# Kernel optimization log

Measured on AMD Instinct MI355X. Metric: run time of the kernel, lower is better.

The kernel has to match this reference:

```python
import jax, jax.numpy as jnp
import numpy as np

N = 50000      # nodes
E = 800000     # edges (avg degree 16)
IN = 128       # in_channels
H = 256        # hidden_channels
EPS = 1e-5     # BatchNorm eps


def setup_inputs() -> dict:
    key = jax.random.key(0)
    ks = iter(jax.random.split(key, 40))
    nrm = lambda shape, s: jax.random.normal(next(ks), shape, dtype=jnp.float32) * s
    d = {}
    d["x"] = nrm((N, IN), 1.0)
    d["edge_index"] = jax.random.randint(next(ks), (2, E), 0, N, dtype=jnp.int32)
    # SAGEConv layers: lin_l (neighbors, with bias) + lin_r (root, no bias); BatchNorm params
    dims = [(IN, H), (H, H), (H, H)]
    for i, (fi, fo) in enumerate(dims):
        s = 1.0 / np.sqrt(fi)
        d[f"w_l{i}"] = nrm((fo, fi), s)
        d[f"b_l{i}"] = nrm((fo,), s)
        d[f"w_r{i}"] = nrm((fo, fi), s)
        d[f"g{i}"] = jnp.ones((fo,), jnp.float32)
        d[f"be{i}"] = nrm((fo,), 0.1)
        d[f"rm{i}"] = nrm((fo,), 0.1)
        d[f"rv{i}"] = jax.random.uniform(next(ks), (fo,), jnp.float32, 0.5, 1.5)
    # predictor MLP: H->H, H->H//2, H//2->1
    for j, (fi, fo) in enumerate([(H, H), (H, H // 2), (H // 2, 1)], start=1):
        s = 1.0 / np.sqrt(fi)
        d[f"pw{j}"] = nrm((fo, fi), s)
        d[f"pb{j}"] = nrm((fo,), s)
    return d


def _sage(x, src, dst, w_l, b_l, w_r):
    # mean aggregation of neighbor messages (gather by src, scatter-add by dst)
    msum = jax.ops.segment_sum(x[src], dst, num_segments=N)       # [N, F]
    cnt = jax.ops.segment_sum(jnp.ones((src.shape[0], 1), x.dtype), dst, num_segments=N)
    mean = msum / jnp.maximum(cnt, 1.0)
    return mean @ w_l.T + b_l + x @ w_r.T


def _bn(x, g, be, rm, rv):
    return (x - rm) * jax.lax.rsqrt(rv + EPS) * g + be


def reference(x, edge_index,
              w_l0, b_l0, w_r0, g0, be0, rm0, rv0,
              w_l1, b_l1, w_r1, g1, be1, rm1, rv1,
              w_l2, b_l2, w_r2, g2, be2, rm2, rv2,
              pw1, pb1, pw2, pb2, pw3, pb3):
    src, dst = edge_index[0], edge_index[1]
    layers = [
        (w_l0, b_l0, w_r0, g0, be0, rm0, rv0),
        (w_l1, b_l1, w_r1, g1, be1, rm1, rv1),
        (w_l2, b_l2, w_r2, g2, be2, rm2, rv2),
    ]
    for (wl, bl, wr, g, be, rm, rv) in layers:
        x = _sage(x, src, dst, wl, bl, wr)
        x = jax.nn.relu(_bn(x, g, be, rm, rv))
        # dropout: identity in eval mode
    h = jax.nn.relu(x @ pw1.T + pb1)
    h = jax.nn.relu(h @ pw2.T + pb2)
    return jax.nn.sigmoid(h @ pw3.T + pb3)   # [N, 1]
```

## Files before the change

### kernel.cpp

```cpp
#include <hip/hip_runtime.h>
#include <hip/hip_fp16.h>

#define NNODES 50000
#define NEDGES 800000

typedef _Float16 f16;
typedef f16 f16x8 __attribute__((ext_vector_type(8)));
typedef f16 f16x4 __attribute__((ext_vector_type(4)));
typedef float f32x4 __attribute__((ext_vector_type(4)));

#define GLOAD_LDS16(g, l) __builtin_amdgcn_global_load_lds( \
    (const __attribute__((address_space(1))) void*)(g), \
    (__attribute__((address_space(3))) void*)(l), 16, 0, 0)


__global__ void k_deg(const int* __restrict__ dst, int* __restrict__ deg, int E) {
    int i = blockIdx.x * blockDim.x + threadIdx.x;
    int stride = gridDim.x * blockDim.x;
    for (; i < E; i += stride) atomicAdd(&deg[dst[i]], 1);
}

__global__ void k_bsum(const int* __restrict__ deg, int* __restrict__ bsum, int n) {
    __shared__ int s[256];
    int i = blockIdx.x * 256 + threadIdx.x;
    s[threadIdx.x] = (i < n) ? ((deg[i] + 7) & ~7) : 0;
    __syncthreads();
    for (int off = 128; off; off >>= 1) {
        if (threadIdx.x < off) s[threadIdx.x] += s[threadIdx.x + off];
        __syncthreads();
    }
    if (threadIdx.x == 0) bsum[blockIdx.x] = s[0];
}

__global__ void k_scan_bsum(int* __restrict__ bsum, int nb) {
    int lane = threadIdx.x & 63;
    int carry = 0;
    for (int base = 0; base < nb; base += 64) {
        int i = base + lane;
        int v = (i < nb) ? bsum[i] : 0;
        int orig = v;
        for (int off = 1; off < 64; off <<= 1) {
            int x = __shfl_up(v, off);
            if (lane >= off) v += x;
        }
        if (i < nb) bsum[i] = carry + v - orig;
        carry += __shfl(v, 63);
    }
}

__global__ void k_offsets(const int* __restrict__ deg, const int* __restrict__ bsum,
                          int* __restrict__ offs, int n) {
    __shared__ int s[256];
    int t = threadIdx.x;
    int i = blockIdx.x * 256 + t;
    int v = (i < n) ? ((deg[i] + 7) & ~7) : 0;
    s[t] = v;
    __syncthreads();
    for (int off = 1; off < 256; off <<= 1) {
        int x = (t >= off) ? s[t - off] : 0;
        __syncthreads();
        s[t] += x;
        __syncthreads();
    }
    if (i < n) offs[i] = bsum[blockIdx.x] + s[t] - v;
    if (i == n - 1) offs[n] = bsum[blockIdx.x] + s[t];
}

__global__ void k_scatter_pad(const int* __restrict__ src, const int* __restrict__ dst,
                              const int* __restrict__ offs, const int* __restrict__ deg,
                              int* __restrict__ cursor, int* __restrict__ csr,
                              int E, int n) {
    int i = blockIdx.x * blockDim.x + threadIdx.x;
    int stride = gridDim.x * blockDim.x;
    for (int e = i; e < E; e += stride) {
        int d = dst[e];
        int p = atomicAdd(&cursor[d], 1);
        csr[offs[d] + p] = src[e];
    }
    for (int v = i; v < n; v += stride) {
        int d = deg[v], pd = (d + 7) & ~7;
        int base = offs[v];
        for (int p = d; p < pd; ++p) csr[base + p] = NNODES;
    }
}


__global__ void k_prep(const float* __restrict__ x, f16* __restrict__ h0, int n4,
                       const float* __restrict__ pw3, f16* __restrict__ pw3f,
                       f16* __restrict__ hA, f16* __restrict__ hB) {
    int gid0 = blockIdx.x * blockDim.x + threadIdx.x;
    int gstride = gridDim.x * blockDim.x;
    for (int i = gid0; i < n4; i += gstride) {
        float4 v = ((const float4*)x)[i];
        f16x4 o;
        o[0] = (f16)v.x; o[1] = (f16)v.y; o[2] = (f16)v.z; o[3] = (f16)v.w;
        ((f16x4*)h0)[i] = o;
    }
    f16x4 z = {};
    if (gid0 < 32) {
        ((f16x4*)(h0 + (size_t)NNODES * 128))[gid0] = z;
    } else if (gid0 < 96) {
        ((f16x4*)(hA + (size_t)NNODES * 256))[gid0 - 32] = z;
    } else if (gid0 < 160) {
        ((f16x4*)(hB + (size_t)NNODES * 256))[gid0 - 96] = z;
    } else if (gid0 < 192) {
        int i = gid0 - 160;
        float4 v = ((const float4*)pw3)[i];
        f16x4 o;
        o[0] = (f16)v.x; o[1] = (f16)v.y; o[2] = (f16)v.z; o[3] = (f16)v.w;
        ((f16x4*)pw3f)[i] = o;
    }
}


#define NPK 8
struct PackSeg { const float* w; f16* p; int FO; int K; };
struct PackArgs { PackSeg s[NPK]; };

__global__ void k_packw(PackArgs a) {
    int gid = blockIdx.x * blockDim.x + threadIdx.x;
    int gstride = gridDim.x * blockDim.x;
    for (int sgi = 0; sgi < NPK; ++sgi) {
        PackSeg sg = a.s[sgi];
        int total = sg.FO * sg.K / 8;
        int KS = sg.K >> 5;
        for (int t = gid; t < total; t += gstride) {
            int lane = t & 63;
            int tile = t >> 6;
            int ks = tile % KS, nt = tile / KS;
            int row = nt * 16 + (lane & 15);
            int col = ks * 32 + (lane >> 4) * 8;
            const float4* src = (const float4*)(sg.w + (size_t)row * sg.K + col);
            float4 v0 = src[0], v1 = src[1];
            f16x8 o;
            o[0] = (f16)v0.x; o[1] = (f16)v0.y; o[2] = (f16)v0.z; o[3] = (f16)v0.w;
            o[4] = (f16)v1.x; o[5] = (f16)v1.y; o[6] = (f16)v1.z; o[7] = (f16)v1.w;
            ((f16x8*)sg.p)[t] = o;
        }
    }
}


struct AffSeg { const float *b, *g, *be, *rm, *rv; float *cs, *cb; int n; int isbn; };
struct AffArgs { AffSeg s[5]; };

__global__ void k_affine_all(AffArgs a) {
    AffSeg sg = a.s[blockIdx.x];
    int t = threadIdx.x;
    if (t < sg.n) {
        if (sg.isbn) {
            float sc = sg.g[t] * rsqrtf(sg.rv[t] + 1e-5f);
            sg.cs[t] = sc;
            sg.cb[t] = (sg.b[t] - sg.rm[t]) * sc + sg.be[t];
        } else {
            sg.cs[t] = 1.0f;
            sg.cb[t] = sg.b[t];
        }
    }
}

template <int F>
__global__ __launch_bounds__(256) void k_aggregate(
    const f16* __restrict__ h, const int* __restrict__ poffs,
    const int* __restrict__ deg, const int* __restrict__ csr,
    f16* __restrict__ mean) {
    constexpr int LPN = F / 8;
    constexpr int NPW = 64 / LPN;
    int tid = threadIdx.x;
    int wave = tid >> 6, lane = tid & 63;
    int node = blockIdx.x * (4 * NPW) + wave * NPW + lane / LPN;
    int t = lane % LPN;
    int beg = poffs[node], end = poffs[node + 1];
    int nb = (end - beg) >> 3;
    const f16x8* hb = (const f16x8*)h;
    float acc[8] = {0.f, 0.f, 0.f, 0.f, 0.f, 0.f, 0.f, 0.f};

    int j = beg;
    for (int p = 0; p + 2 <= nb; p += 2, j += 16) {
        int iA[8], iB[8];
#pragma unroll
        for (int u = 0; u < 8; ++u) iA[u] = csr[j + u];
#pragma unroll
        for (int u = 0; u < 8; ++u) iB[u] = csr[j + 8 + u];
        f16x8 vA[8], vB[8];
#pragma unroll
        for (int u = 0; u < 8; ++u) vA[u] = hb[(size_t)iA[u] * LPN + t];
#pragma unroll
        for (int u = 0; u < 8; ++u) vB[u] = hb[(size_t)iB[u] * LPN + t];
#pragma unroll
        for (int u = 0; u < 8; ++u)
#pragma unroll
            for (int e = 0; e < 8; ++e) acc[e] += (float)vA[u][e];
#pragma unroll
        for (int u = 0; u < 8; ++u)
#pragma unroll
            for (int e = 0; e < 8; ++e) acc[e] += (float)vB[u][e];
    }
    if (nb & 1) {
        int iA[8];
#pragma unroll
        for (int u = 0; u < 8; ++u) iA[u] = csr[j + u];
        f16x8 vA[8];
#pragma unroll
        for (int u = 0; u < 8; ++u) vA[u] = hb[(size_t)iA[u] * LPN + t];
#pragma unroll
        for (int u = 0; u < 8; ++u)
#pragma unroll
            for (int e = 0; e < 8; ++e) acc[e] += (float)vA[u][e];
    }

    int d = deg[node];
    float inv = (d > 0) ? 1.0f / (float)d : 0.0f;
    f16x8 o;
#pragma unroll
    for (int e = 0; e < 8; ++e) o[e] = (f16)(acc[e] * inv);
    ((f16x8*)mean)[(size_t)node * LPN + t] = o;
}

template <int FO, bool FUSE>
__global__ __launch_bounds__(FO * 2, 4) void k_gemm(
    const f16* __restrict__ A1, const f16* __restrict__ A2,
    const f16* __restrict__ W1p, const f16* __restrict__ W2p,
    const float* __restrict__ cs, const float* __restrict__ cb,
    f16* __restrict__ out, const f16* __restrict__ w3,
    const float* __restrict__ pb3, float* __restrict__ outF,
    int M, int K) {
    constexpr int WC = FO / 64;
    constexpr int NT = FO * 2;
    __shared__ f16 As[2][128 * 64];
    __shared__ float smF[WC][128];
    int tid = threadIdx.x;
    int lane = tid & 63;
    int wave = tid >> 6;
    int wr = wave / WC, wc = wave % WC;
    int m0 = blockIdx.x * 128;
    int lrow = lane & 15;
    int kof8 = (lane >> 4) * 8;
    int KC1 = K >> 6;
    int KS = K >> 5;
    int NC = A2 ? KC1 * 2 : KC1;

    auto stage = [&](int buf, int c) {
        int ph = (c >= KC1) ? 1 : 0;
        const char* Ab = (const char*)(ph ? A2 : A1);
        int kb0 = ((c - ph * KC1) << 6) * 2;
        char* Al = (char*)&As[buf][0];
#pragma unroll
        for (int u0 = 0; u0 < 1024; u0 += NT) {
            int u = u0 + tid;
            int row = u >> 3;
            int kb = (u & 7) * 16;
            int grow = m0 + row; if (grow > M - 1) grow = M - 1;
            GLOAD_LDS16(Ab + (size_t)grow * (K * 2) + kb0 + (kb ^ ((row & 7) << 4)), Al + u * 16);
        }
    };

    f32x4 acc[4][4] = {};

    stage(0, 0);
    __syncthreads();

    for (int c = 0; c < NC; ++c) {
        int ph = (c >= KC1) ? 1 : 0;
        const f16x8* Wp = (const f16x8*)(ph ? W2p : W1p);
        int cl = c - ph * KC1;
        f16x8 b[2][4];
#pragma unroll
        for (int kk = 0; kk < 2; ++kk) {
            int ks = cl * 2 + kk;
#pragma unroll
            for (int ni = 0; ni < 4; ++ni) {
                int nt = wc * 4 + ni;
                b[kk][ni] = Wp[((size_t)nt * KS + ks) * 64 + lane];
            }
        }
        if (c + 1 < NC) stage((c + 1) & 1, c + 1);
        const char* Al = (const char*)&As[c & 1][0];
#pragma unroll
        for (int kk = 0; kk < 2; ++kk) {
            int kb = kof8 * 2 + kk * 64;
            f16x8 a[4];
#pragma unroll
            for (int mi = 0; mi < 4; ++mi) {
                int r = wr * 64 + mi * 16 + lrow;
                a[mi] = *(const f16x8*)(Al + r * 128 + (kb ^ ((r & 7) << 4)));
            }
#pragma unroll
            for (int mi = 0; mi < 4; ++mi)
#pragma unroll
                for (int ni = 0; ni < 4; ++ni)
                    acc[mi][ni] = __builtin_amdgcn_mfma_f32_16x16x32_f16(a[mi], b[kk][ni], acc[mi][ni], 0, 0, 0);
        }
        __syncthreads();
    }

    if constexpr (!FUSE) {
        int rquad = (lane >> 4) * 4;
#pragma unroll
        for (int mi = 0; mi < 4; ++mi) {
#pragma unroll
            for (int ni = 0; ni < 4; ++ni) {
                int col = wc * 64 + ni * 16 + (lane & 15);
                float s = cs[col], cc = cb[col];
#pragma unroll
                for (int r = 0; r < 4; ++r) {
                    int row = m0 + wr * 64 + mi * 16 + rquad + r;
                    if (row < M) {
                        float v = acc[mi][ni][r] * s + cc;
                        v = fmaxf(v, 0.f);
                        out[(size_t)row * FO + col] = (f16)v;
                    }
                }
            }
        }
    } else {
        float b3 = pb3[0];
        float rsum[4][4] = {};
#pragma unroll
        for (int ni = 0; ni < 4; ++ni) {
            int col = wc * 64 + ni * 16 + (lane & 15);
            float w3v = (float)w3[col];
            float cbv = cb[col];
#pragma unroll
            for (int mi = 0; mi < 4; ++mi)
#pragma unroll
                for (int r = 0; r < 4; ++r)
                    rsum[mi][r] += fmaxf(acc[mi][ni][r] + cbv, 0.f) * w3v;
        }
#pragma unroll
        for (int mi = 0; mi < 4; ++mi)
#pragma unroll
            for (int r = 0; r < 4; ++r) {
                float s = rsum[mi][r];
                s += __shfl_xor(s, 1); s += __shfl_xor(s, 2);
                s += __shfl_xor(s, 4); s += __shfl_xor(s, 8);
                if ((lane & 15) == 0)
                    smF[wc][wr * 64 + mi * 16 + (lane >> 4) * 4 + r] = s;
            }
        __syncthreads();
        if (tid < 128) {
            int row = m0 + tid;
            if (row < M) {
                float s = b3;
#pragma unroll
                for (int w = 0; w < WC; ++w) s += smF[w][tid];
                outF[row] = 1.0f / (1.0f + expf(-s));
            }
        }
    }
}


extern "C" void kernel_launch(void* const* d_in, const int* in_sizes, int n_in,
                              void* d_out, int out_size, void* d_ws, size_t ws_size,
                              hipStream_t stream) {
    const float* x = (const float*)d_in[0];
    const int* ei = (const int*)d_in[1];
    const int* src = ei;
    const int* dst = ei + NEDGES;
    const float* w_l[3] = {(const float*)d_in[2], (const float*)d_in[9], (const float*)d_in[16]};
    const float* b_l[3] = {(const float*)d_in[3], (const float*)d_in[10], (const float*)d_in[17]};
    const float* w_r[3] = {(const float*)d_in[4], (const float*)d_in[11], (const float*)d_in[18]};
    const float* g[3]  = {(const float*)d_in[5], (const float*)d_in[12], (const float*)d_in[19]};
    const float* be[3] = {(const float*)d_in[6], (const float*)d_in[13], (const float*)d_in[20]};
    const float* rm[3] = {(const float*)d_in[7], (const float*)d_in[14], (const float*)d_in[21]};
    const float* rv[3] = {(const float*)d_in[8], (const float*)d_in[15], (const float*)d_in[22]};
    const float* pw1 = (const float*)d_in[23]; const float* pb1 = (const float*)d_in[24];
    const float* pw2 = (const float*)d_in[25]; const float* pb2 = (const float*)d_in[26];
    const float* pw3 = (const float*)d_in[27]; const float* pb3 = (const float*)d_in[28];

    char* wsb = (char*)d_ws;
    size_t o = 0;
    auto alloc = [&](size_t b) { size_t r = o; o = (o + b + 255) & ~(size_t)255; return r; };

    size_t deg_off = alloc(NNODES * 4);
    size_t cur_off = alloc(NNODES * 4);
    int* deg    = (int*)(wsb + deg_off);
    int* cursor = (int*)(wsb + cur_off);
    int* poffs  = (int*)(wsb + alloc((NNODES + 1) * 4));
    int* bsum   = (int*)(wsb + alloc(256 * 4));
    int* csr    = (int*)(wsb + alloc((NEDGES + 8 * NNODES) * 4));
    f16* h0   = (f16*)(wsb + alloc((size_t)(NNODES + 1) * 128 * 2));
    f16* hA   = (f16*)(wsb + alloc((size_t)(NNODES + 1) * 256 * 2));
    f16* hB   = (f16*)(wsb + alloc((size_t)(NNODES + 1) * 256 * 2));
    f16* mean = (f16*)(wsb + alloc((size_t)NNODES * 256 * 2));
    f16* wl0p = (f16*)(wsb + alloc(256 * 128 * 2));
    f16* wr0p = (f16*)(wsb + alloc(256 * 128 * 2));
    f16* wl1p = (f16*)(wsb + alloc(256 * 256 * 2));
    f16* wr1p = (f16*)(wsb + alloc(256 * 256 * 2));
    f16* wl2p = (f16*)(wsb + alloc(256 * 256 * 2));
    f16* wr2p = (f16*)(wsb + alloc(256 * 256 * 2));
    f16* pw1p = (f16*)(wsb + alloc(256 * 256 * 2));
    f16* pw2p = (f16*)(wsb + alloc(128 * 256 * 2));
    f16* pw3f = (f16*)(wsb + alloc(128 * 2));
    float* csv[5]; float* cbv[5];
    for (int i = 0; i < 5; ++i) {
        csv[i] = (float*)(wsb + alloc(256 * 4));
        cbv[i] = (float*)(wsb + alloc(256 * 4));
    }

    hipMemsetAsync(wsb + deg_off, 0, cur_off - deg_off + NNODES * 4, stream);
    k_deg<<<3125, 256, 0, stream>>>(dst, deg, NEDGES);
    int nb = (NNODES + 255) / 256;
    k_bsum<<<nb, 256, 0, stream>>>(deg, bsum, NNODES);
    k_scan_bsum<<<1, 64, 0, stream>>>(bsum, nb);
    k_offsets<<<nb, 256, 0, stream>>>(deg, bsum, poffs, NNODES);
    k_scatter_pad<<<3125, 256, 0, stream>>>(src, dst, poffs, deg, cursor, csr, NEDGES, NNODES);

    k_prep<<<1600, 256, 0, stream>>>(x, h0, NNODES * 128 / 4, pw3, pw3f, hA, hB);
    PackArgs pa;
    pa.s[0] = {w_l[0], wl0p, 256, 128};
    pa.s[1] = {w_r[0], wr0p, 256, 128};
    pa.s[2] = {w_l[1], wl1p, 256, 256};
    pa.s[3] = {w_r[1], wr1p, 256, 256};
    pa.s[4] = {w_l[2], wl2p, 256, 256};
    pa.s[5] = {w_r[2], wr2p, 256, 256};
    pa.s[6] = {pw1,    pw1p, 256, 256};
    pa.s[7] = {pw2,    pw2p, 128, 256};
    k_packw<<<64, 256, 0, stream>>>(pa);

    AffArgs aa;
    for (int i = 0; i < 3; ++i)
        aa.s[i] = {b_l[i], g[i], be[i], rm[i], rv[i], csv[i], cbv[i], 256, 1};
    aa.s[3] = {pb1, nullptr, nullptr, nullptr, nullptr, csv[3], cbv[3], 256, 0};
    aa.s[4] = {pb2, nullptr, nullptr, nullptr, nullptr, csv[4], cbv[4], 128, 0};
    k_affine_all<<<5, 256, 0, stream>>>(aa);

    int gm = (NNODES + 127) / 128;

    k_aggregate<128><<<3125, 256, 0, stream>>>(h0, poffs, deg, csr, mean);
    k_gemm<256, false><<<gm, 512, 0, stream>>>(mean, h0, wl0p, wr0p, csv[0], cbv[0], hA,
                                               nullptr, nullptr, nullptr, NNODES, 128);
    k_aggregate<256><<<6250, 256, 0, stream>>>(hA, poffs, deg, csr, mean);
    k_gemm<256, false><<<gm, 512, 0, stream>>>(mean, hA, wl1p, wr1p, csv[1], cbv[1], hB,
                                               nullptr, nullptr, nullptr, NNODES, 256);
    k_aggregate<256><<<6250, 256, 0, stream>>>(hB, poffs, deg, csr, mean);
    k_gemm<256, false><<<gm, 512, 0, stream>>>(mean, hB, wl2p, wr2p, csv[2], cbv[2], hA,
                                               nullptr, nullptr, nullptr, NNODES, 256);
    k_gemm<256, false><<<gm, 512, 0, stream>>>(hA, nullptr, pw1p, nullptr, csv[3], cbv[3], hB,
                                               nullptr, nullptr, nullptr, NNODES, 256);
    k_gemm<128, true><<<gm, 256, 0, stream>>>(hB, nullptr, pw2p, nullptr, csv[4], cbv[4], nullptr,
                                              pw3f, pb3, (float*)d_out, NNODES, 256);
}
```

Measured before the change: 347.0 us.

## Fuse preprocessing kernels into one launch and split 256-wide GEMMs across two blocks

The degree count, input cast, weight packing, BN affine folding and padding-row init now run in a single k_front launch, with each role picked by block index. This removes several small kernel launches. The FO=256 GEMMs now use 256-thread blocks, each covering 128 output columns, so the grid doubles to about 782 blocks for better CU occupancy. The cost is that each A tile is now loaded into LDS twice, once per column half.

```diff
diff --git a/kernel.cpp b/kernel.cpp
--- a/kernel.cpp
+++ b/kernel.cpp
@@ -13,12 +13,6 @@
     (const __attribute__((address_space(1))) void*)(g), \
     (__attribute__((address_space(3))) void*)(l), 16, 0, 0)
 
-
-__global__ void k_deg(const int* __restrict__ dst, int* __restrict__ deg, int E) {
-    int i = blockIdx.x * blockDim.x + threadIdx.x;
-    int stride = gridDim.x * blockDim.x;
-    for (; i < E; i += stride) atomicAdd(&deg[dst[i]], 1);
-}
 
 __global__ void k_bsum(const int* __restrict__ deg, int* __restrict__ bsum, int n) {
     __shared__ int s[256];
@@ -85,76 +79,78 @@
 }
 
 
-__global__ void k_prep(const float* __restrict__ x, f16* __restrict__ h0, int n4,
-                       const float* __restrict__ pw3, f16* __restrict__ pw3f,
-                       f16* __restrict__ hA, f16* __restrict__ hB) {
-    int gid0 = blockIdx.x * blockDim.x + threadIdx.x;
-    int gstride = gridDim.x * blockDim.x;
-    for (int i = gid0; i < n4; i += gstride) {
-        float4 v = ((const float4*)x)[i];
-        f16x4 o;
-        o[0] = (f16)v.x; o[1] = (f16)v.y; o[2] = (f16)v.z; o[3] = (f16)v.w;
-        ((f16x4*)h0)[i] = o;
-    }
-    f16x4 z = {};
-    if (gid0 < 32) {
-        ((f16x4*)(h0 + (size_t)NNODES * 128))[gid0] = z;
-    } else if (gid0 < 96) {
-        ((f16x4*)(hA + (size_t)NNODES * 256))[gid0 - 32] = z;
-    } else if (gid0 < 160) {
-        ((f16x4*)(hB + (size_t)NNODES * 256))[gid0 - 96] = z;
-    } else if (gid0 < 192) {
-        int i = gid0 - 160;
-        float4 v = ((const float4*)pw3)[i];
-        f16x4 o;
-        o[0] = (f16)v.x; o[1] = (f16)v.y; o[2] = (f16)v.z; o[3] = (f16)v.w;
-        ((f16x4*)pw3f)[i] = o;
-    }
-}
-
-
 #define NPK 8
 struct PackSeg { const float* w; f16* p; int FO; int K; };
-struct PackArgs { PackSeg s[NPK]; };
-
-__global__ void k_packw(PackArgs a) {
-    int gid = blockIdx.x * blockDim.x + threadIdx.x;
-    int gstride = gridDim.x * blockDim.x;
-    for (int sgi = 0; sgi < NPK; ++sgi) {
-        PackSeg sg = a.s[sgi];
-        int total = sg.FO * sg.K / 8;
-        int KS = sg.K >> 5;
-        for (int t = gid; t < total; t += gstride) {
-            int lane = t & 63;
-            int tile = t >> 6;
-            int ks = tile % KS, nt = tile / KS;
-            int row = nt * 16 + (lane & 15);
-            int col = ks * 32 + (lane >> 4) * 8;
-            const float4* src = (const float4*)(sg.w + (size_t)row * sg.K + col);
-            float4 v0 = src[0], v1 = src[1];
-            f16x8 o;
-            o[0] = (f16)v0.x; o[1] = (f16)v0.y; o[2] = (f16)v0.z; o[3] = (f16)v0.w;
-            o[4] = (f16)v1.x; o[5] = (f16)v1.y; o[6] = (f16)v1.z; o[7] = (f16)v1.w;
-            ((f16x8*)sg.p)[t] = o;
-        }
-    }
-}
-
-
 struct AffSeg { const float *b, *g, *be, *rm, *rv; float *cs, *cb; int n; int isbn; };
-struct AffArgs { AffSeg s[5]; };
-
-__global__ void k_affine_all(AffArgs a) {
-    AffSeg sg = a.s[blockIdx.x];
-    int t = threadIdx.x;
-    if (t < sg.n) {
-        if (sg.isbn) {
-            float sc = sg.g[t] * rsqrtf(sg.rv[t] + 1e-5f);
-            sg.cs[t] = sc;
-            sg.cb[t] = (sg.b[t] - sg.rm[t]) * sc + sg.be[t];
-        } else {
-            sg.cs[t] = 1.0f;
-            sg.cb[t] = sg.b[t];
+
+struct FrontArgs {
+    const int* dst; int* deg;
+    const float* x; f16* h0; int n4;
+    const float* pw3; f16* pw3f;
+    f16 *hA, *hB;
+    PackSeg ps[NPK];
+    AffSeg as[5];
+};
+
+__global__ void k_front(FrontArgs a) {
+    int b = blockIdx.x, tid = threadIdx.x;
+    if (b < 1024) {
+        int i = b * 256 + tid, stride = 1024 * 256;
+        for (; i < NEDGES; i += stride) atomicAdd(&a.deg[a.dst[i]], 1);
+    } else if (b < 2624) {
+        int i = (b - 1024) * 256 + tid, stride = 1600 * 256;
+        for (; i < a.n4; i += stride) {
+            float4 v = ((const float4*)a.x)[i];
+            f16x4 o;
+            o[0] = (f16)v.x; o[1] = (f16)v.y; o[2] = (f16)v.z; o[3] = (f16)v.w;
+            ((f16x4*)a.h0)[i] = o;
+        }
+    } else if (b < 2880) {
+        int gid = (b - 2624) * 256 + tid, gstride = 256 * 256;
+        for (int sgi = 0; sgi < NPK; ++sgi) {
+            PackSeg sg = a.ps[sgi];
+            int total = sg.FO * sg.K / 8;
+            int KS = sg.K >> 5;
+            for (int t = gid; t < total; t += gstride) {
+                int lane = t & 63;
+                int tile = t >> 6;
+                int ks = tile % KS, nt = tile / KS;
+                int row = nt * 16 + (lane & 15);
+                int col = ks * 32 + (lane >> 4) * 8;
+                const float4* srcp = (const float4*)(sg.w + (size_t)row * sg.K + col);
+                float4 v0 = srcp[0], v1 = srcp[1];
+                f16x8 o;
+                o[0] = (f16)v0.x; o[1] = (f16)v0.y; o[2] = (f16)v0.z; o[3] = (f16)v0.w;
+                o[4] = (f16)v1.x; o[5] = (f16)v1.y; o[6] = (f16)v1.z; o[7] = (f16)v1.w;
+                ((f16x8*)sg.p)[t] = o;
+            }
+        }
+    } else if (b < 2885) {
+        AffSeg sg = a.as[b - 2880];
+        if (tid < sg.n) {
+            if (sg.isbn) {
+                float sc = sg.g[tid] * rsqrtf(sg.rv[tid] + 1e-5f);
+                sg.cs[tid] = sc;
+                sg.cb[tid] = (sg.b[tid] - sg.rm[tid]) * sc + sg.be[tid];
+            } else {
+                sg.cs[tid] = 1.0f;
+                sg.cb[tid] = sg.b[tid];
+            }
+        }
+    } else {
+        f16x4 z = {};
+        if (tid < 32) {
+            ((f16x4*)(a.h0 + (size_t)NNODES * 128))[tid] = z;
+        } else if (tid < 96) {
+            ((f16x4*)(a.hA + (size_t)NNODES * 256))[tid - 32] = z;
+        } else if (tid < 160) {
+            ((f16x4*)(a.hB + (size_t)NNODES * 256))[tid - 96] = z;
+        } else if (tid < 192) {
+            int i = tid - 160;
+            float4 v = ((const float4*)a.pw3)[i];
+            f16x4 o;
+            o[0] = (f16)v.x; o[1] = (f16)v.y; o[2] = (f16)v.z; o[3] = (f16)v.w;
+            ((f16x4*)a.pw3f)[i] = o;
         }
     }
 }
@@ -217,16 +213,105 @@
     ((f16x8*)mean)[(size_t)node * LPN + t] = o;
 }
 
-template <int FO, bool FUSE>
-__global__ __launch_bounds__(FO * 2, 4) void k_gemm(
+__global__ __launch_bounds__(256, 4) void k_gemm2(
     const f16* __restrict__ A1, const f16* __restrict__ A2,
     const f16* __restrict__ W1p, const f16* __restrict__ W2p,
     const float* __restrict__ cs, const float* __restrict__ cb,
-    f16* __restrict__ out, const f16* __restrict__ w3,
+    f16* __restrict__ out, int M, int K) {
+    __shared__ f16 As[2][128 * 64];
+    int tid = threadIdx.x;
+    int lane = tid & 63;
+    int wave = tid >> 6;
+    int wr = wave >> 1, wc = wave & 1;
+    int m0 = (blockIdx.x >> 1) * 128;
+    int nb0 = (blockIdx.x & 1) * 128;
+    int lrow = lane & 15;
+    int kof8 = (lane >> 4) * 8;
+    int KC1 = K >> 6;
+    int KS = K >> 5;
+    int NC = A2 ? KC1 * 2 : KC1;
+
+    auto stage = [&](int buf, int c) {
+        int ph = (c >= KC1) ? 1 : 0;
+        const char* Ab = (const char*)(ph ? A2 : A1);
+        int kb0 = ((c - ph * KC1) << 6) * 2;
+        char* Al = (char*)&As[buf][0];
+#pragma unroll
+        for (int u0 = 0; u0 < 1024; u0 += 256) {
+            int u = u0 + tid;
+            int row = u >> 3;
+            int kb = (u & 7) * 16;
+            int grow = m0 + row; if (grow > M - 1) grow = M - 1;
+            GLOAD_LDS16(Ab + (size_t)grow * (K * 2) + kb0 + (kb ^ ((row & 7) << 4)), Al + u * 16);
+        }
+    };
+
+    f32x4 acc[4][4] = {};
+
+    stage(0, 0);
+    __syncthreads();
+
+    for (int c = 0; c < NC; ++c) {
+        int ph = (c >= KC1) ? 1 : 0;
+        const f16x8* Wp = (const f16x8*)(ph ? W2p : W1p);
+        int cl = c - ph * KC1;
+        f16x8 b[2][4];
+#pragma unroll
+        for (int kk = 0; kk < 2; ++kk) {
+            int ks = cl * 2 + kk;
+#pragma unroll
+            for (int ni = 0; ni < 4; ++ni) {
+                int nt = (nb0 >> 4) + wc * 4 + ni;
+                b[kk][ni] = Wp[((size_t)nt * KS + ks) * 64 + lane];
+            }
+        }
+        if (c + 1 < NC) stage((c + 1) & 1, c + 1);
+        const char* Al = (const char*)&As[c & 1][0];
+#pragma unroll
+        for (int kk = 0; kk < 2; ++kk) {
+            int kb = kof8 * 2 + kk * 64;
+            f16x8 a[4];
+#pragma unroll
+            for (int mi = 0; mi < 4; ++mi) {
+                int r = wr * 64 + mi * 16 + lrow;
+                a[mi] = *(const f16x8*)(Al + r * 128 + (kb ^ ((r & 7) << 4)));
+            }
+#pragma unroll
+            for (int mi = 0; mi < 4; ++mi)
+#pragma unroll
+                for (int ni = 0; ni < 4; ++ni)
+                    acc[mi][ni] = __builtin_amdgcn_mfma_f32_16x16x32_f16(a[mi], b[kk][ni], acc[mi][ni], 0, 0, 0);
+        }
+        __syncthreads();
+    }
+
+    int rquad = (lane >> 4) * 4;
+#pragma unroll
+    for (int mi = 0; mi < 4; ++mi) {
+#pragma unroll
+        for (int ni = 0; ni < 4; ++ni) {
+            int col = nb0 + wc * 64 + ni * 16 + lrow;
+            float s = cs[col], cc = cb[col];
+#pragma unroll
+            for (int r = 0; r < 4; ++r) {
+                int row = m0 + wr * 64 + mi * 16 + rquad + r;
+                if (row < M) {
+                    float v = acc[mi][ni][r] * s + cc;
+                    v = fmaxf(v, 0.f);
+                    out[(size_t)row * 256 + col] = (f16)v;
+                }
+            }
+        }
+    }
+}
+
+__global__ __launch_bounds__(256, 4) void k_gemmF(
+    const f16* __restrict__ A1, const f16* __restrict__ W1p,
+    const float* __restrict__ cb, const f16* __restrict__ w3,
     const float* __restrict__ pb3, float* __restrict__ outF,
     int M, int K) {
-    constexpr int WC = FO / 64;
-    constexpr int NT = FO * 2;
+    constexpr int FO = 128;
+    constexpr int WC = 2;
     __shared__ f16 As[2][128 * 64];
     __shared__ float smF[WC][128];
     int tid = threadIdx.x;
@@ -238,20 +323,18 @@
     int kof8 = (lane >> 4) * 8;
     int KC1 = K >> 6;
     int KS = K >> 5;
-    int NC = A2 ? KC1 * 2 : KC1;
+    int NC = KC1;
 
     auto stage = [&](int buf, int c) {
-        int ph = (c >= KC1) ? 1 : 0;
-        const char* Ab = (const char*)(ph ? A2 : A1);
-        int kb0 = ((c - ph * KC1) << 6) * 2;
+        int kb0 = (c << 6) * 2;
         char* Al = (char*)&As[buf][0];
 #pragma unroll
-        for (int u0 = 0; u0 < 1024; u0 += NT) {
+        for (int u0 = 0; u0 < 1024; u0 += 256) {
             int u = u0 + tid;
             int row = u >> 3;
             int kb = (u & 7) * 16;
             int grow = m0 + row; if (grow > M - 1) grow = M - 1;
-            GLOAD_LDS16(Ab + (size_t)grow * (K * 2) + kb0 + (kb ^ ((row & 7) << 4)), Al + u * 16);
+            GLOAD_LDS16((const char*)A1 + (size_t)grow * (K * 2) + kb0 + (kb ^ ((row & 7) << 4)), Al + u * 16);
         }
     };
 
@@ -261,13 +344,11 @@
     __syncthreads();
 
     for (int c = 0; c < NC; ++c) {
-        int ph = (c >= KC1) ? 1 : 0;
-        const f16x8* Wp = (const f16x8*)(ph ? W2p : W1p);
-        int cl = c - ph * KC1;
+        const f16x8* Wp = (const f16x8*)W1p;
         f16x8 b[2][4];
 #pragma unroll
         for (int kk = 0; kk < 2; ++kk) {
-            int ks = cl * 2 + kk;
+            int ks = c * 2 + kk;
 #pragma unroll
             for (int ni = 0; ni < 4; ++ni) {
                 int nt = wc * 4 + ni;
@@ -294,58 +375,35 @@
         __syncthreads();
     }
 
-    if constexpr (!FUSE) {
-        int rquad = (lane >> 4) * 4;
-#pragma unroll
-        for (int mi = 0; mi < 4; ++mi) {
-#pragma unroll
-            for (int ni = 0; ni < 4; ++ni) {
-                int col = wc * 64 + ni * 16 + (lane & 15);
-                float s = cs[col], cc = cb[col];
-#pragma unroll
-                for (int r = 0; r < 4; ++r) {
-                    int row = m0 + wr * 64 + mi * 16 + rquad + r;
-                    if (row < M) {
-                        float v = acc[mi][ni][r] * s + cc;
-                        v = fmaxf(v, 0.f);
-                        out[(size_t)row * FO + col] = (f16)v;
-                    }
-                }
-            }
-        }
-    } else {
-        float b3 = pb3[0];
-        float rsum[4][4] = {};
-#pragma unroll
-        for (int ni = 0; ni < 4; ++ni) {
-            int col = wc * 64 + ni * 16 + (lane & 15);
-            float w3v = (float)w3[col];
-            float cbv = cb[col];
-#pragma unroll
-            for (int mi = 0; mi < 4; ++mi)
-#pragma unroll
-                for (int r = 0; r < 4; ++r)
-                    rsum[mi][r] += fmaxf(acc[mi][ni][r] + cbv, 0.f) * w3v;
-        }
+    float b3 = pb3[0];
+    float rsum[4][4] = {};
+#pragma unroll
+    for (int ni = 0; ni < 4; ++ni) {
+        int col = wc * 64 + ni * 16 + lrow;
+        float w3v = (float)w3[col];
+        float cbv = cb[col];
 #pragma unroll
         for (int mi = 0; mi < 4; ++mi)
 #pragma unroll
-            for (int r = 0; r < 4; ++r) {
-                float s = rsum[mi][r];
-                s += __shfl_xor(s, 1); s += __shfl_xor(s, 2);
-                s += __shfl_xor(s, 4); s += __shfl_xor(s, 8);
-                if ((lane & 15) == 0)
-                    smF[wc][wr * 64 + mi * 16 + (lane >> 4) * 4 + r] = s;
-            }
-        __syncthreads();
-        if (tid < 128) {
-            int row = m0 + tid;
-            if (row < M) {
-                float s = b3;
-#pragma unroll
-                for (int w = 0; w < WC; ++w) s += smF[w][tid];
-                outF[row] = 1.0f / (1.0f + expf(-s));
-            }
+            for (int r = 0; r < 4; ++r)
+                rsum[mi][r] += fmaxf(acc[mi][ni][r] + cbv, 0.f) * w3v;
+    }
+#pragma unroll
+    for (int mi = 0; mi < 4; ++mi)
+#pragma unroll
+        for (int r = 0; r < 4; ++r) {
+            float s = rsum[mi][r];
+            s += __shfl_xor(s, 1); s += __shfl_xor(s, 2);
+            s += __shfl_xor(s, 4); s += __shfl_xor(s, 8);
+            if ((lane & 15) == 0)
+                smF[wc][wr * 64 + mi * 16 + (lane >> 4) * 4 + r] = s;
+        }
+    __syncthreads();
+    if (tid < 128) {
+        int row = m0 + tid;
+        if (row < M) {
+            float s = smF[0][tid] + smF[1][tid] + b3;
+            outF[row] = 1.0f / (1.0f + expf(-s));
         }
     }
 }
@@ -400,45 +458,40 @@
     }
 
     hipMemsetAsync(wsb + deg_off, 0, cur_off - deg_off + NNODES * 4, stream);
-    k_deg<<<3125, 256, 0, stream>>>(dst, deg, NEDGES);
+    FrontArgs fa;
+    fa.dst = dst; fa.deg = deg;
+    fa.x = x; fa.h0 = h0; fa.n4 = NNODES * 128 / 4;
+    fa.pw3 = pw3; fa.pw3f = pw3f;
+    fa.hA = hA; fa.hB = hB;
+    fa.ps[0] = {w_l[0], wl0p, 256, 128};
+    fa.ps[1] = {w_r[0], wr0p, 256, 128};
+    fa.ps[2] = {w_l[1], wl1p, 256, 256};
+    fa.ps[3] = {w_r[1], wr1p, 256, 256};
+    fa.ps[4] = {w_l[2], wl2p, 256, 256};
+    fa.ps[5] = {w_r[2], wr2p, 256, 256};
+    fa.ps[6] = {pw1,    pw1p, 256, 256};
+    fa.ps[7] = {pw2,    pw2p, 128, 256};
+    for (int i = 0; i < 3; ++i)
+        fa.as[i] = {b_l[i], g[i], be[i], rm[i], rv[i], csv[i], cbv[i], 256, 1};
+    fa.as[3] = {pb1, nullptr, nullptr, nullptr, nullptr, csv[3], cbv[3], 256, 0};
+    fa.as[4] = {pb2, nullptr, nullptr, nullptr, nullptr, csv[4], cbv[4], 128, 0};
+    k_front<<<2886, 256, 0, stream>>>(fa);
+
     int nb = (NNODES + 255) / 256;
     k_bsum<<<nb, 256, 0, stream>>>(deg, bsum, NNODES);
     k_scan_bsum<<<1, 64, 0, stream>>>(bsum, nb);
     k_offsets<<<nb, 256, 0, stream>>>(deg, bsum, poffs, NNODES);
     k_scatter_pad<<<3125, 256, 0, stream>>>(src, dst, poffs, deg, cursor, csr, NEDGES, NNODES);
 
-    k_prep<<<1600, 256, 0, stream>>>(x, h0, NNODES * 128 / 4, pw3, pw3f, hA, hB);
-    PackArgs pa;
-    pa.s[0] = {w_l[0], wl0p, 256, 128};
-    pa.s[1] = {w_r[0], wr0p, 256, 128};
-    pa.s[2] = {w_l[1], wl1p, 256, 256};
-    pa.s[3] = {w_r[1], wr1p, 256, 256};
-    pa.s[4] = {w_l[2], wl2p, 256, 256};
-    pa.s[5] = {w_r[2], wr2p, 256, 256};
-    pa.s[6] = {pw1,    pw1p, 256, 256};
-    pa.s[7] = {pw2,    pw2p, 128, 256};
-    k_packw<<<64, 256, 0, stream>>>(pa);
-
-    AffArgs aa;
-    for (int i = 0; i < 3; ++i)
-        aa.s[i] = {b_l[i], g[i], be[i], rm[i], rv[i], csv[i], cbv[i], 256, 1};
-    aa.s[3] = {pb1, nullptr, nullptr, nullptr, nullptr, csv[3], cbv[3], 256, 0};
-    aa.s[4] = {pb2, nullptr, nullptr, nullptr, nullptr, csv[4], cbv[4], 128, 0};
-    k_affine_all<<<5, 256, 0, stream>>>(aa);
-
-    int gm = (NNODES + 127) / 128;
+    int gm2 = ((NNODES + 127) / 128) * 2;
+    int gmF = (NNODES + 127) / 128;
 
     k_aggregate<128><<<3125, 256, 0, stream>>>(h0, poffs, deg, csr, mean);
-    k_gemm<256, false><<<gm, 512, 0, stream>>>(mean, h0, wl0p, wr0p, csv[0], cbv[0], hA,
-                                               nullptr, nullptr, nullptr, NNODES, 128);
+    k_gemm2<<<gm2, 256, 0, stream>>>(mean, h0, wl0p, wr0p, csv[0], cbv[0], hA, NNODES, 128);
     k_aggregate<256><<<6250, 256, 0, stream>>>(hA, poffs, deg, csr, mean);
-    k_gemm<256, false><<<gm, 512, 0, stream>>>(mean, hA, wl1p, wr1p, csv[1], cbv[1], hB,
-                                               nullptr, nullptr, nullptr, NNODES, 256);
+    k_gemm2<<<gm2, 256, 0, stream>>>(mean, hA, wl1p, wr1p, csv[1], cbv[1], hB, NNODES, 256);
     k_aggregate<256><<<6250, 256, 0, stream>>>(hB, poffs, deg, csr, mean);
-    k_gemm<256, false><<<gm, 512, 0, stream>>>(mean, hB, wl2p, wr2p, csv[2], cbv[2], hA,
-                                               nullptr, nullptr, nullptr, NNODES, 256);
-    k_gemm<256, false><<<gm, 512, 0, stream>>>(hA, nullptr, pw1p, nullptr, csv[3], cbv[3], hB,
-                                               nullptr, nullptr, nullptr, NNODES, 256);
-    k_gemm<128, true><<<gm, 256, 0, stream>>>(hB, nullptr, pw2p, nullptr, csv[4], cbv[4], nullptr,
-                                              pw3f, pb3, (float*)d_out, NNODES, 256);
-}
+    k_gemm2<<<gm2, 256, 0, stream>>>(mean, hB, wl2p, wr2p, csv[2], cbv[2], hA, NNODES, 256);
+    k_gemm2<<<gm2, 256, 0, stream>>>(hA, nullptr, pw1p, nullptr, csv[3], cbv[3], hB, NNODES, 256);
+    k_gemmF<<<gmF, 256, 0, stream>>>(hB, pw2p, cbv[4], pw3f, pb3, (float*)d_out, NNODES, 256);
+}
```

Measured after the change: 364.6 us. 1.05x slower.
